# Kernel tuning notes

Hardware: AMD Instinct MI355X
Metric: run time of the kernel (lower is better)

## Reference

```python
import jax, jax.numpy as jnp
import numpy as np

QUERY_SIZE = 512
KEY_SIZE = 512
VALUE_SIZE = 512
HIDDEN = 128


def setup_inputs() -> dict:
    key = jax.random.key(0)
    ks = jax.random.split(key, 9)
    b, t_q, t_k = 8, 128, 512
    query = jax.random.normal(ks[0], (b, t_q, QUERY_SIZE), dtype=jnp.float32)
    keys = jax.random.normal(ks[1], (b, t_k, KEY_SIZE), dtype=jnp.float32)
    values = jax.random.normal(ks[2], (b, t_k, VALUE_SIZE), dtype=jnp.float32)
    # torch nn.Linear init ~ U(-1/sqrt(fan_in), 1/sqrt(fan_in)); scale-matched normals are fine
    sq = 1.0 / np.sqrt(QUERY_SIZE)
    sk = 1.0 / np.sqrt(KEY_SIZE)
    sh = 1.0 / np.sqrt(HIDDEN)
    Wq = jax.random.uniform(ks[3], (HIDDEN, QUERY_SIZE), jnp.float32, -sq, sq)
    bq = jax.random.uniform(ks[4], (HIDDEN,), jnp.float32, -sq, sq)
    Wk = jax.random.uniform(ks[5], (HIDDEN, KEY_SIZE), jnp.float32, -sk, sk)
    bk = jax.random.uniform(ks[6], (HIDDEN,), jnp.float32, -sk, sk)
    Wo = jax.random.uniform(ks[7], (1, HIDDEN), jnp.float32, -sh, sh)
    bo = jax.random.uniform(ks[8], (1,), jnp.float32, -sh, sh)
    return {"query": query, "keys": keys, "values": values,
            "Wq": Wq, "bq": bq, "Wk": Wk, "bk": bk, "Wo": Wo, "bo": bo}


def reference(query, keys, values, Wq, bq, Wk, bk, Wo, bo):
    # Bahdanau additive attention: att_ij = Wo @ tanh(Wq q_i + Wk k_j + bq + bk) + bo
    # Project once per position (mathematically identical to the expanded per-pair Linear).
    q_proj = jnp.einsum('bqn,hn->bqh', query, Wq) + bq          # b x t_q x h
    k_proj = jnp.einsum('bkn,hn->bkh', keys, Wk) + bk           # b x t_k x h
    hid = jnp.tanh(q_proj[:, :, None, :] + k_proj[:, None, :, :])  # b x t_q x t_k x h
    scores = jnp.einsum('bqkh,h->bqk', hid, Wo[0]) + bo[0]       # b x t_q x t_k
    attn = jax.nn.softmax(scores, axis=2)
    context = jnp.einsum('bqk,bkv->bqv', attn, values)           # b x t_q x n_v
    return context, attn
```

## Files before the change

kernel.cpp:

```cpp
#include <hip/hip_runtime.h>


#define B_    8
#define TQ_   128
#define TK_   512
#define NIN_  512
#define H_    128
#define NV_   512
#define NQR   (B_*TQ_)
#define NROWS (NQR + B_*TK_)

#define C2_   2.8853900817779268f
#define L2E_  1.4426950408889634f

__device__ __forceinline__ float fexp2(float x){ return __builtin_amdgcn_exp2f(x); }
__device__ __forceinline__ float frcp (float x){ return __builtin_amdgcn_rcpf(x); }

__global__ __launch_bounds__(128, 4) void proj_kernel(
        const float* __restrict__ query, const float* __restrict__ keys,
        const float* __restrict__ Wq, const float* __restrict__ Wk,
        float* __restrict__ psum, int kper) {
    __shared__ float at[32][20];
    __shared__ float wt[32][132];
    const int tid = threadIdx.x;
    const int r0  = blockIdx.x * 16;
    const float* in; const float* W;
    if (r0 < NQR) { in = query + (size_t)r0 * NIN_;         W = Wq; }
    else          { in = keys  + (size_t)(r0 - NQR) * NIN_; W = Wk; }

    const int r4 = (tid >> 5) * 4;
    const int h4 = (tid & 31) * 4;
    const int sr  = tid >> 3;
    const int skq = (tid & 7) * 4;
    const int kb0 = blockIdx.y * kper;
    const int nc  = kper >> 5;

    const float* pA = in + sr * NIN_ + kb0 + skq;
    const float* pW0 = W + (sr      ) * NIN_ + kb0 + skq;
    const float* pW1 = W + (sr + 16 ) * NIN_ + kb0 + skq;
    const float* pW2 = W + (sr + 32 ) * NIN_ + kb0 + skq;
    const float* pW3 = W + (sr + 48 ) * NIN_ + kb0 + skq;
    const float* pW4 = W + (sr + 64 ) * NIN_ + kb0 + skq;
    const float* pW5 = W + (sr + 80 ) * NIN_ + kb0 + skq;
    const float* pW6 = W + (sr + 96 ) * NIN_ + kb0 + skq;
    const float* pW7 = W + (sr + 112) * NIN_ + kb0 + skq;

    float4 af  = *(const float4*)pA;
    float4 w0 = *(const float4*)pW0, w1 = *(const float4*)pW1;
    float4 w2 = *(const float4*)pW2, w3 = *(const float4*)pW3;
    float4 w4 = *(const float4*)pW4, w5 = *(const float4*)pW5;
    float4 w6 = *(const float4*)pW6, w7 = *(const float4*)pW7;

    float acc[4][4];
#pragma unroll
    for (int i = 0; i < 4; ++i)
#pragma unroll
        for (int j = 0; j < 4; ++j) acc[i][j] = 0.0f;

    for (int c = 0; c < nc; ++c) {
        __syncthreads();
        at[skq+0][sr] = af.x; at[skq+1][sr] = af.y;
        at[skq+2][sr] = af.z; at[skq+3][sr] = af.w;
        wt[skq+0][sr    ] = w0.x; wt[skq+1][sr    ] = w0.y;
        wt[skq+2][sr    ] = w0.z; wt[skq+3][sr    ] = w0.w;
        wt[skq+0][sr+ 16] = w1.x; wt[skq+1][sr+ 16] = w1.y;
        wt[skq+2][sr+ 16] = w1.z; wt[skq+3][sr+ 16] = w1.w;
        wt[skq+0][sr+ 32] = w2.x; wt[skq+1][sr+ 32] = w2.y;
        wt[skq+2][sr+ 32] = w2.z; wt[skq+3][sr+ 32] = w2.w;
        wt[skq+0][sr+ 48] = w3.x; wt[skq+1][sr+ 48] = w3.y;
        wt[skq+2][sr+ 48] = w3.z; wt[skq+3][sr+ 48] = w3.w;
        wt[skq+0][sr+ 64] = w4.x; wt[skq+1][sr+ 64] = w4.y;
        wt[skq+2][sr+ 64] = w4.z; wt[skq+3][sr+ 64] = w4.w;
        wt[skq+0][sr+ 80] = w5.x; wt[skq+1][sr+ 80] = w5.y;
        wt[skq+2][sr+ 80] = w5.z; wt[skq+3][sr+ 80] = w5.w;
        wt[skq+0][sr+ 96] = w6.x; wt[skq+1][sr+ 96] = w6.y;
        wt[skq+2][sr+ 96] = w6.z; wt[skq+3][sr+ 96] = w6.w;
        wt[skq+0][sr+112] = w7.x; wt[skq+1][sr+112] = w7.y;
        wt[skq+2][sr+112] = w7.z; wt[skq+3][sr+112] = w7.w;
        __syncthreads();
        if (c + 1 < nc) {
            pA += 32; pW0 += 32; pW1 += 32; pW2 += 32; pW3 += 32;
            pW4 += 32; pW5 += 32; pW6 += 32; pW7 += 32;
            af = *(const float4*)pA;
            w0 = *(const float4*)pW0; w1 = *(const float4*)pW1;
            w2 = *(const float4*)pW2; w3 = *(const float4*)pW3;
            w4 = *(const float4*)pW4; w5 = *(const float4*)pW5;
            w6 = *(const float4*)pW6; w7 = *(const float4*)pW7;
        }
#pragma unroll 8
        for (int kk = 0; kk < 32; ++kk) {
            float4 a = *(const float4*)&at[kk][r4];
            float4 w = *(const float4*)&wt[kk][h4];
            float av[4] = {a.x, a.y, a.z, a.w};
            float wv[4] = {w.x, w.y, w.z, w.w};
#pragma unroll
            for (int i = 0; i < 4; ++i)
#pragma unroll
                for (int j = 0; j < 4; ++j)
                    acc[i][j] = fmaf(av[i], wv[j], acc[i][j]);
        }
    }

    float* op = psum + ((size_t)blockIdx.y * NROWS + r0) * H_;
#pragma unroll
    for (int i = 0; i < 4; ++i) {
        float4 o = {acc[i][0], acc[i][1], acc[i][2], acc[i][3]};
        *(float4*)&op[(r4 + i) * H_ + h4] = o;
    }
}

__global__ __launch_bounds__(256, 4) void reduce_kernel(
        const float* __restrict__ psum, const float* __restrict__ bq,
        const float* __restrict__ bk, float* __restrict__ qp,
        float* __restrict__ kpT) {
    __shared__ float lt[128][9];
    const int tid = threadIdx.x;
    const int r0  = blockIdx.x * 8;
    const bool isq = (r0 < NQR);
    const float* bias = isq ? bq : bk;

    const int row = tid >> 5, hq = (tid & 31) * 4;
    const float4 b4 = *(const float4*)&bias[hq];
    float4 s = b4;
#pragma unroll
    for (int sp = 0; sp < 4; ++sp) {
        float4 v = *(const float4*)&psum[((size_t)sp * NROWS + r0 + row) * H_ + hq];
        s.x += v.x; s.y += v.y; s.z += v.z; s.w += v.w;
    }
    if (isq) {
        *(float4*)&qp[(size_t)(r0 + row) * H_ + hq] = s;
    } else {
        lt[hq + 0][row] = s.x * C2_; lt[hq + 1][row] = s.y * C2_;
        lt[hq + 2][row] = s.z * C2_; lt[hq + 3][row] = s.w * C2_;
        __syncthreads();
        const int b  = (r0 - NQR) >> 9;
        const int k0 = (r0 - NQR) & 511;
        const int h = tid >> 1, kq = (tid & 1) * 4;
        float4 o = {lt[h][kq], lt[h][kq + 1], lt[h][kq + 2], lt[h][kq + 3]};
        *(float4*)&kpT[((size_t)b * H_ + h) * TK_ + k0 + kq] = o;
    }
}

__global__ __launch_bounds__(256, 4) void scores_kernel(
        const float* __restrict__ qp, const float* __restrict__ kpT,
        const float* __restrict__ Wo, const float* __restrict__ bo,
        float* __restrict__ out_attn) {
    __shared__ float qs2[2][H_];
    __shared__ float w2[H_];
    __shared__ float sc[2][TK_];

    const int tid = threadIdx.x;
    const int b   = blockIdx.y;
    const int q0  = blockIdx.x * 2;
    const int lane = tid & 63;

    qs2[tid >> 7][tid & 127] =
        qp[(b * TQ_ + q0 + (tid >> 7)) * H_ + (tid & 127)] * C2_;
    if (tid < H_) w2[tid] = Wo[tid] * -2.0f;
    __syncthreads();

    float sw = w2[lane] + w2[lane + 64];
#pragma unroll
    for (int m = 1; m < 64; m <<= 1) sw += __shfl_xor(sw, m);
    const float sbase = bo[0] - 0.5f * sw;

    const int k4 = (tid & 127) * 4;
    const int qi = tid >> 7;
    const float* pk = kpT + (size_t)b * H_ * TK_ + k4;
    float a0 = 0.f, a1 = 0.f, a2 = 0.f, a3 = 0.f;
#pragma unroll 4
    for (int h = 0; h < H_; ++h) {
        float4 kv = *(const float4*)pk;
        pk += TK_;
        const float qv = qs2[qi][h];
        const float wv = w2[h];
        a0 = fmaf(wv, frcp(fexp2(qv + kv.x) + 1.0f), a0);
        a1 = fmaf(wv, frcp(fexp2(qv + kv.y) + 1.0f), a1);
        a2 = fmaf(wv, frcp(fexp2(qv + kv.z) + 1.0f), a2);
        a3 = fmaf(wv, frcp(fexp2(qv + kv.w) + 1.0f), a3);
    }
    float4 sv = {a0 + sbase, a1 + sbase, a2 + sbase, a3 + sbase};
    *(float4*)&sc[qi][k4] = sv;
    __syncthreads();

    const int w = tid >> 6;
    if (w < 2) {
        float4 sA = *(const float4*)&sc[w][lane * 8];
        float4 sB = *(const float4*)&sc[w][lane * 8 + 4];
        float m = fmaxf(fmaxf(fmaxf(sA.x, sA.y), fmaxf(sA.z, sA.w)),
                        fmaxf(fmaxf(sB.x, sB.y), fmaxf(sB.z, sB.w)));
#pragma unroll
        for (int mask = 1; mask < 64; mask <<= 1) m = fmaxf(m, __shfl_xor(m, mask));
        float4 eA, eB;
        eA.x = fexp2((sA.x - m) * L2E_); eA.y = fexp2((sA.y - m) * L2E_);
        eA.z = fexp2((sA.z - m) * L2E_); eA.w = fexp2((sA.w - m) * L2E_);
        eB.x = fexp2((sB.x - m) * L2E_); eB.y = fexp2((sB.y - m) * L2E_);
        eB.z = fexp2((sB.z - m) * L2E_); eB.w = fexp2((sB.w - m) * L2E_);
        float s = eA.x + eA.y + eA.z + eA.w + eB.x + eB.y + eB.z + eB.w;
#pragma unroll
        for (int mask = 1; mask < 64; mask <<= 1) s += __shfl_xor(s, mask);
        float inv = frcp(s);
        eA.x *= inv; eA.y *= inv; eA.z *= inv; eA.w *= inv;
        eB.x *= inv; eB.y *= inv; eB.z *= inv; eB.w *= inv;
        float4* op = (float4*)&out_attn[(b * TQ_ + q0 + w) * TK_ + lane * 8];
        op[0] = eA; op[1] = eB;
    }
}

__global__ __launch_bounds__(128, 4) void context_kernel(
        const float* __restrict__ attn, const float* __restrict__ values,
        float* __restrict__ outc) {
    __shared__ float at[32][12];
    __shared__ float vt[32][68];

    const int tid = threadIdx.x;
    const int b   = blockIdx.y;
    const int q0  = (blockIdx.x >> 3) * 8;
    const int v0  = (blockIdx.x & 7) * 64;

    const int v2 = (tid & 31) * 2;
    const int q2 = (tid >> 5) * 2;
    const int ar  = tid >> 3;
    const int akq = (tid & 7) * 4;
    const int vr  = tid >> 4;
    const int vq  = (tid & 15) * 4;

    const float* pAt = attn + (size_t)(b * TQ_ + q0 + ar) * TK_ + akq;
    const float* pV0 = values + (size_t)(b * TK_ + vr     ) * NV_ + v0 + vq;
    const float* pV1 = values + (size_t)(b * TK_ + vr +  8) * NV_ + v0 + vq;
    const float* pV2 = values + (size_t)(b * TK_ + vr + 16) * NV_ + v0 + vq;
    const float* pV3 = values + (size_t)(b * TK_ + vr + 24) * NV_ + v0 + vq;

    float4 af = {0.f,0.f,0.f,0.f};
    if (tid < 64) af = *(const float4*)pAt;
    float4 vf0 = *(const float4*)pV0;
    float4 vf1 = *(const float4*)pV1;
    float4 vf2 = *(const float4*)pV2;
    float4 vf3 = *(const float4*)pV3;

    float acc[2][2] = {{0.f,0.f},{0.f,0.f}};

    for (int c = 0; c < 16; ++c) {
        __syncthreads();
        if (tid < 64) {
            at[akq+0][ar] = af.x; at[akq+1][ar] = af.y;
            at[akq+2][ar] = af.z; at[akq+3][ar] = af.w;
        }
        *(float4*)&vt[vr     ][vq] = vf0;
        *(float4*)&vt[vr +  8][vq] = vf1;
        *(float4*)&vt[vr + 16][vq] = vf2;
        *(float4*)&vt[vr + 24][vq] = vf3;
        __syncthreads();
        if (c + 1 < 16) {
            pAt += 32; pV0 += 32 * NV_; pV1 += 32 * NV_;
            pV2 += 32 * NV_; pV3 += 32 * NV_;
            if (tid < 64) af = *(const float4*)pAt;
            vf0 = *(const float4*)pV0; vf1 = *(const float4*)pV1;
            vf2 = *(const float4*)pV2; vf3 = *(const float4*)pV3;
        }
#pragma unroll 8
        for (int kk = 0; kk < 32; ++kk) {
            float2 a = *(const float2*)&at[kk][q2];
            float2 v = *(const float2*)&vt[kk][v2];
            acc[0][0] = fmaf(a.x, v.x, acc[0][0]);
            acc[0][1] = fmaf(a.x, v.y, acc[0][1]);
            acc[1][0] = fmaf(a.y, v.x, acc[1][0]);
            acc[1][1] = fmaf(a.y, v.y, acc[1][1]);
        }
    }
    float2 o0 = {acc[0][0], acc[0][1]};
    float2 o1 = {acc[1][0], acc[1][1]};
    *(float2*)&outc[(size_t)(b * TQ_ + q0 + q2 + 0) * NV_ + v0 + v2] = o0;
    *(float2*)&outc[(size_t)(b * TQ_ + q0 + q2 + 1) * NV_ + v0 + v2] = o1;
}

extern "C" void kernel_launch(void* const* d_in, const int* in_sizes, int n_in,
                              void* d_out, int out_size, void* d_ws, size_t ws_size,
                              hipStream_t stream) {
    const float* query  = (const float*)d_in[0];
    const float* keys   = (const float*)d_in[1];
    const float* values = (const float*)d_in[2];
    const float* Wq     = (const float*)d_in[3];
    const float* bq     = (const float*)d_in[4];
    const float* Wk     = (const float*)d_in[5];
    const float* bk     = (const float*)d_in[6];
    const float* Wo     = (const float*)d_in[7];
    const float* bo     = (const float*)d_in[8];

    float* out_ctx  = (float*)d_out;
    float* out_attn = out_ctx + B_ * TQ_ * NV_;
    float* qp   = (float*)d_ws;
    float* kpT  = qp + (size_t)NQR * H_;
    float* psum = kpT + (size_t)B_ * H_ * TK_;

    proj_kernel<<<dim3(NROWS / 16, 4), 128, 0, stream>>>(
        query, keys, Wq, Wk, psum, NIN_ / 4);
    reduce_kernel<<<NROWS / 8, 256, 0, stream>>>(psum, bq, bk, qp, kpT);
    scores_kernel<<<dim3(TQ_ / 2, B_), 256, 0, stream>>>(qp, kpT, Wo, bo, out_attn);
    context_kernel<<<dim3(128, B_), 128, 0, stream>>>(out_attn, values, out_ctx);
}
```

Measured before the change: 69.17 us.

## Drop split-K reduce kernel, fuse bias into projection, row-major key layout in scores

The projection kernel no longer splits the 512-wide reduction four ways. Each block now computes the full K for 16 rows and 64 hidden units, then adds the bias and C2 scale directly, so the separate reduce kernel and its partial-sum traffic are gone. Keys are stored row-major and not transposed. The scores kernel now has each thread handle one key with both queries, reading contiguous float4s of kp and broadcast q and w from shared memory. The cost is fewer, longer projection blocks, and strided per-thread kp reads in scores that may coalesce poorly.

```diff
diff --git a/kernel.cpp b/kernel.cpp
--- a/kernel.cpp
+++ b/kernel.cpp
@@ -18,131 +18,86 @@
 
 __global__ __launch_bounds__(128, 4) void proj_kernel(
         const float* __restrict__ query, const float* __restrict__ keys,
-        const float* __restrict__ Wq, const float* __restrict__ Wk,
-        float* __restrict__ psum, int kper) {
+        const float* __restrict__ Wq, const float* __restrict__ bq,
+        const float* __restrict__ Wk, const float* __restrict__ bk,
+        float* __restrict__ qp, float* __restrict__ kp) {
     __shared__ float at[32][20];
-    __shared__ float wt[32][132];
+    __shared__ float wt[32][68];
     const int tid = threadIdx.x;
-    const int r0  = blockIdx.x * 16;
-    const float* in; const float* W;
-    if (r0 < NQR) { in = query + (size_t)r0 * NIN_;         W = Wq; }
-    else          { in = keys  + (size_t)(r0 - NQR) * NIN_; W = Wk; }
-
-    const int r4 = (tid >> 5) * 4;
-    const int h4 = (tid & 31) * 4;
+    const int r0  = (blockIdx.x >> 1) * 16;
+    const int h0  = (blockIdx.x & 1) * 64;
+    const float* in; const float* W; const float* bias; float* outp;
+    if (r0 < NQR) {
+        in = query + (size_t)r0 * NIN_; W = Wq; bias = bq;
+        outp = qp + (size_t)r0 * H_;
+    } else {
+        const int rk = r0 - NQR;
+        in = keys + (size_t)rk * NIN_;  W = Wk; bias = bk;
+        outp = kp + (size_t)rk * H_;
+    }
+
+    const int r2  = (tid >> 4) * 2;
+    const int h4l = (tid & 15) * 4;
     const int sr  = tid >> 3;
     const int skq = (tid & 7) * 4;
-    const int kb0 = blockIdx.y * kper;
-    const int nc  = kper >> 5;
-
-    const float* pA = in + sr * NIN_ + kb0 + skq;
-    const float* pW0 = W + (sr      ) * NIN_ + kb0 + skq;
-    const float* pW1 = W + (sr + 16 ) * NIN_ + kb0 + skq;
-    const float* pW2 = W + (sr + 32 ) * NIN_ + kb0 + skq;
-    const float* pW3 = W + (sr + 48 ) * NIN_ + kb0 + skq;
-    const float* pW4 = W + (sr + 64 ) * NIN_ + kb0 + skq;
-    const float* pW5 = W + (sr + 80 ) * NIN_ + kb0 + skq;
-    const float* pW6 = W + (sr + 96 ) * NIN_ + kb0 + skq;
-    const float* pW7 = W + (sr + 112) * NIN_ + kb0 + skq;
-
-    float4 af  = *(const float4*)pA;
+
+    const float* pA  = in + (size_t)sr * NIN_ + skq;
+    const float* pW0 = W + (size_t)(h0 + sr     ) * NIN_ + skq;
+    const float* pW1 = W + (size_t)(h0 + sr + 16) * NIN_ + skq;
+    const float* pW2 = W + (size_t)(h0 + sr + 32) * NIN_ + skq;
+    const float* pW3 = W + (size_t)(h0 + sr + 48) * NIN_ + skq;
+
+    float4 af = *(const float4*)pA;
     float4 w0 = *(const float4*)pW0, w1 = *(const float4*)pW1;
     float4 w2 = *(const float4*)pW2, w3 = *(const float4*)pW3;
-    float4 w4 = *(const float4*)pW4, w5 = *(const float4*)pW5;
-    float4 w6 = *(const float4*)pW6, w7 = *(const float4*)pW7;
-
-    float acc[4][4];
-#pragma unroll
-    for (int i = 0; i < 4; ++i)
-#pragma unroll
-        for (int j = 0; j < 4; ++j) acc[i][j] = 0.0f;
-
-    for (int c = 0; c < nc; ++c) {
+
+    float acc[2][4] = {{0.f,0.f,0.f,0.f},{0.f,0.f,0.f,0.f}};
+
+    for (int c = 0; c < 16; ++c) {
         __syncthreads();
         at[skq+0][sr] = af.x; at[skq+1][sr] = af.y;
         at[skq+2][sr] = af.z; at[skq+3][sr] = af.w;
-        wt[skq+0][sr    ] = w0.x; wt[skq+1][sr    ] = w0.y;
-        wt[skq+2][sr    ] = w0.z; wt[skq+3][sr    ] = w0.w;
-        wt[skq+0][sr+ 16] = w1.x; wt[skq+1][sr+ 16] = w1.y;
-        wt[skq+2][sr+ 16] = w1.z; wt[skq+3][sr+ 16] = w1.w;
-        wt[skq+0][sr+ 32] = w2.x; wt[skq+1][sr+ 32] = w2.y;
-        wt[skq+2][sr+ 32] = w2.z; wt[skq+3][sr+ 32] = w2.w;
-        wt[skq+0][sr+ 48] = w3.x; wt[skq+1][sr+ 48] = w3.y;
-        wt[skq+2][sr+ 48] = w3.z; wt[skq+3][sr+ 48] = w3.w;
-        wt[skq+0][sr+ 64] = w4.x; wt[skq+1][sr+ 64] = w4.y;
-        wt[skq+2][sr+ 64] = w4.z; wt[skq+3][sr+ 64] = w4.w;
-        wt[skq+0][sr+ 80] = w5.x; wt[skq+1][sr+ 80] = w5.y;
-        wt[skq+2][sr+ 80] = w5.z; wt[skq+3][sr+ 80] = w5.w;
-        wt[skq+0][sr+ 96] = w6.x; wt[skq+1][sr+ 96] = w6.y;
-        wt[skq+2][sr+ 96] = w6.z; wt[skq+3][sr+ 96] = w6.w;
-        wt[skq+0][sr+112] = w7.x; wt[skq+1][sr+112] = w7.y;
-        wt[skq+2][sr+112] = w7.z; wt[skq+3][sr+112] = w7.w;
-        __syncthreads();
-        if (c + 1 < nc) {
+        wt[skq+0][sr   ] = w0.x; wt[skq+1][sr   ] = w0.y;
+        wt[skq+2][sr   ] = w0.z; wt[skq+3][sr   ] = w0.w;
+        wt[skq+0][sr+16] = w1.x; wt[skq+1][sr+16] = w1.y;
+        wt[skq+2][sr+16] = w1.z; wt[skq+3][sr+16] = w1.w;
+        wt[skq+0][sr+32] = w2.x; wt[skq+1][sr+32] = w2.y;
+        wt[skq+2][sr+32] = w2.z; wt[skq+3][sr+32] = w2.w;
+        wt[skq+0][sr+48] = w3.x; wt[skq+1][sr+48] = w3.y;
+        wt[skq+2][sr+48] = w3.z; wt[skq+3][sr+48] = w3.w;
+        __syncthreads();
+        if (c + 1 < 16) {
             pA += 32; pW0 += 32; pW1 += 32; pW2 += 32; pW3 += 32;
-            pW4 += 32; pW5 += 32; pW6 += 32; pW7 += 32;
             af = *(const float4*)pA;
             w0 = *(const float4*)pW0; w1 = *(const float4*)pW1;
             w2 = *(const float4*)pW2; w3 = *(const float4*)pW3;
-            w4 = *(const float4*)pW4; w5 = *(const float4*)pW5;
-            w6 = *(const float4*)pW6; w7 = *(const float4*)pW7;
         }
 #pragma unroll 8
         for (int kk = 0; kk < 32; ++kk) {
-            float4 a = *(const float4*)&at[kk][r4];
-            float4 w = *(const float4*)&wt[kk][h4];
-            float av[4] = {a.x, a.y, a.z, a.w};
-            float wv[4] = {w.x, w.y, w.z, w.w};
-#pragma unroll
-            for (int i = 0; i < 4; ++i)
-#pragma unroll
-                for (int j = 0; j < 4; ++j)
-                    acc[i][j] = fmaf(av[i], wv[j], acc[i][j]);
-        }
-    }
-
-    float* op = psum + ((size_t)blockIdx.y * NROWS + r0) * H_;
-#pragma unroll
-    for (int i = 0; i < 4; ++i) {
-        float4 o = {acc[i][0], acc[i][1], acc[i][2], acc[i][3]};
-        *(float4*)&op[(r4 + i) * H_ + h4] = o;
-    }
-}
-
-__global__ __launch_bounds__(256, 4) void reduce_kernel(
-        const float* __restrict__ psum, const float* __restrict__ bq,
-        const float* __restrict__ bk, float* __restrict__ qp,
-        float* __restrict__ kpT) {
-    __shared__ float lt[128][9];
-    const int tid = threadIdx.x;
-    const int r0  = blockIdx.x * 8;
-    const bool isq = (r0 < NQR);
-    const float* bias = isq ? bq : bk;
-
-    const int row = tid >> 5, hq = (tid & 31) * 4;
-    const float4 b4 = *(const float4*)&bias[hq];
-    float4 s = b4;
-#pragma unroll
-    for (int sp = 0; sp < 4; ++sp) {
-        float4 v = *(const float4*)&psum[((size_t)sp * NROWS + r0 + row) * H_ + hq];
-        s.x += v.x; s.y += v.y; s.z += v.z; s.w += v.w;
-    }
-    if (isq) {
-        *(float4*)&qp[(size_t)(r0 + row) * H_ + hq] = s;
-    } else {
-        lt[hq + 0][row] = s.x * C2_; lt[hq + 1][row] = s.y * C2_;
-        lt[hq + 2][row] = s.z * C2_; lt[hq + 3][row] = s.w * C2_;
-        __syncthreads();
-        const int b  = (r0 - NQR) >> 9;
-        const int k0 = (r0 - NQR) & 511;
-        const int h = tid >> 1, kq = (tid & 1) * 4;
-        float4 o = {lt[h][kq], lt[h][kq + 1], lt[h][kq + 2], lt[h][kq + 3]};
-        *(float4*)&kpT[((size_t)b * H_ + h) * TK_ + k0 + kq] = o;
+            const float2 a = *(const float2*)&at[kk][r2];
+            const float4 w = *(const float4*)&wt[kk][h4l];
+            acc[0][0] = fmaf(a.x, w.x, acc[0][0]);
+            acc[0][1] = fmaf(a.x, w.y, acc[0][1]);
+            acc[0][2] = fmaf(a.x, w.z, acc[0][2]);
+            acc[0][3] = fmaf(a.x, w.w, acc[0][3]);
+            acc[1][0] = fmaf(a.y, w.x, acc[1][0]);
+            acc[1][1] = fmaf(a.y, w.y, acc[1][1]);
+            acc[1][2] = fmaf(a.y, w.z, acc[1][2]);
+            acc[1][3] = fmaf(a.y, w.w, acc[1][3]);
+        }
+    }
+
+    const float4 b4 = *(const float4*)&bias[h0 + h4l];
+#pragma unroll
+    for (int i = 0; i < 2; ++i) {
+        float4 o = {(acc[i][0] + b4.x) * C2_, (acc[i][1] + b4.y) * C2_,
+                    (acc[i][2] + b4.z) * C2_, (acc[i][3] + b4.w) * C2_};
+        *(float4*)&outp[(size_t)(r2 + i) * H_ + h0 + h4l] = o;
     }
 }
 
 __global__ __launch_bounds__(256, 4) void scores_kernel(
-        const float* __restrict__ qp, const float* __restrict__ kpT,
+        const float* __restrict__ qp, const float* __restrict__ kp,
         const float* __restrict__ Wo, const float* __restrict__ bo,
         float* __restrict__ out_attn) {
     __shared__ float qs2[2][H_];
@@ -155,7 +110,7 @@
     const int lane = tid & 63;
 
     qs2[tid >> 7][tid & 127] =
-        qp[(b * TQ_ + q0 + (tid >> 7)) * H_ + (tid & 127)] * C2_;
+        qp[(size_t)(b * TQ_ + q0 + (tid >> 7)) * H_ + (tid & 127)];
     if (tid < H_) w2[tid] = Wo[tid] * -2.0f;
     __syncthreads();
 
@@ -164,23 +119,29 @@
     for (int m = 1; m < 64; m <<= 1) sw += __shfl_xor(sw, m);
     const float sbase = bo[0] - 0.5f * sw;
 
-    const int k4 = (tid & 127) * 4;
-    const int qi = tid >> 7;
-    const float* pk = kpT + (size_t)b * H_ * TK_ + k4;
-    float a0 = 0.f, a1 = 0.f, a2 = 0.f, a3 = 0.f;
+#pragma unroll
+    for (int half = 0; half < 2; ++half) {
+        const int k = tid + half * 256;
+        const float4* kp4 = (const float4*)&kp[(size_t)(b * TK_ + k) * H_];
+        float s0 = 0.f, s1 = 0.f;
 #pragma unroll 4
-    for (int h = 0; h < H_; ++h) {
-        float4 kv = *(const float4*)pk;
-        pk += TK_;
-        const float qv = qs2[qi][h];
-        const float wv = w2[h];
-        a0 = fmaf(wv, frcp(fexp2(qv + kv.x) + 1.0f), a0);
-        a1 = fmaf(wv, frcp(fexp2(qv + kv.y) + 1.0f), a1);
-        a2 = fmaf(wv, frcp(fexp2(qv + kv.z) + 1.0f), a2);
-        a3 = fmaf(wv, frcp(fexp2(qv + kv.w) + 1.0f), a3);
-    }
-    float4 sv = {a0 + sbase, a1 + sbase, a2 + sbase, a3 + sbase};
-    *(float4*)&sc[qi][k4] = sv;
+        for (int hb = 0; hb < 32; ++hb) {
+            const float4 kv  = kp4[hb];
+            const float4 wv  = *(const float4*)&w2[hb * 4];
+            const float4 q0v = *(const float4*)&qs2[0][hb * 4];
+            const float4 q1v = *(const float4*)&qs2[1][hb * 4];
+            s0 = fmaf(wv.x, frcp(fexp2(q0v.x + kv.x) + 1.f), s0);
+            s0 = fmaf(wv.y, frcp(fexp2(q0v.y + kv.y) + 1.f), s0);
+            s0 = fmaf(wv.z, frcp(fexp2(q0v.z + kv.z) + 1.f), s0);
+            s0 = fmaf(wv.w, frcp(fexp2(q0v.w + kv.w) + 1.f), s0);
+            s1 = fmaf(wv.x, frcp(fexp2(q1v.x + kv.x) + 1.f), s1);
+            s1 = fmaf(wv.y, frcp(fexp2(q1v.y + kv.y) + 1.f), s1);
+            s1 = fmaf(wv.z, frcp(fexp2(q1v.z + kv.z) + 1.f), s1);
+            s1 = fmaf(wv.w, frcp(fexp2(q1v.w + kv.w) + 1.f), s1);
+        }
+        sc[0][k] = s0 + sbase;
+        sc[1][k] = s1 + sbase;
+    }
     __syncthreads();
 
     const int w = tid >> 6;
@@ -190,7 +151,7 @@
         float m = fmaxf(fmaxf(fmaxf(sA.x, sA.y), fmaxf(sA.z, sA.w)),
                         fmaxf(fmaxf(sB.x, sB.y), fmaxf(sB.z, sB.w)));
 #pragma unroll
-        for (int mask = 1; mask < 64; mask <<= 1) m = fmaxf(m, __shfl_xor(m, mask));
+        for (int mk = 1; mk < 64; mk <<= 1) m = fmaxf(m, __shfl_xor(m, mk));
         float4 eA, eB;
         eA.x = fexp2((sA.x - m) * L2E_); eA.y = fexp2((sA.y - m) * L2E_);
         eA.z = fexp2((sA.z - m) * L2E_); eA.w = fexp2((sA.w - m) * L2E_);
@@ -198,11 +159,11 @@
         eB.z = fexp2((sB.z - m) * L2E_); eB.w = fexp2((sB.w - m) * L2E_);
         float s = eA.x + eA.y + eA.z + eA.w + eB.x + eB.y + eB.z + eB.w;
 #pragma unroll
-        for (int mask = 1; mask < 64; mask <<= 1) s += __shfl_xor(s, mask);
-        float inv = frcp(s);
+        for (int mk = 1; mk < 64; mk <<= 1) s += __shfl_xor(s, mk);
+        const float inv = frcp(s);
         eA.x *= inv; eA.y *= inv; eA.z *= inv; eA.w *= inv;
         eB.x *= inv; eB.y *= inv; eB.z *= inv; eB.w *= inv;
-        float4* op = (float4*)&out_attn[(b * TQ_ + q0 + w) * TK_ + lane * 8];
+        float4* op = (float4*)&out_attn[(size_t)(b * TQ_ + q0 + w) * TK_ + lane * 8];
         op[0] = eA; op[1] = eB;
     }
 }
@@ -260,8 +221,8 @@
         }
 #pragma unroll 8
         for (int kk = 0; kk < 32; ++kk) {
-            float2 a = *(const float2*)&at[kk][q2];
-            float2 v = *(const float2*)&vt[kk][v2];
+            const float2 a = *(const float2*)&at[kk][q2];
+            const float2 v = *(const float2*)&vt[kk][v2];
             acc[0][0] = fmaf(a.x, v.x, acc[0][0]);
             acc[0][1] = fmaf(a.x, v.y, acc[0][1]);
             acc[1][0] = fmaf(a.y, v.x, acc[1][0]);
@@ -289,13 +250,11 @@
 
     float* out_ctx  = (float*)d_out;
     float* out_attn = out_ctx + B_ * TQ_ * NV_;
-    float* qp   = (float*)d_ws;
-    float* kpT  = qp + (size_t)NQR * H_;
-    float* psum = kpT + (size_t)B_ * H_ * TK_;
-
-    proj_kernel<<<dim3(NROWS / 16, 4), 128, 0, stream>>>(
-        query, keys, Wq, Wk, psum, NIN_ / 4);
-    reduce_kernel<<<NROWS / 8, 256, 0, stream>>>(psum, bq, bk, qp, kpT);
-    scores_kernel<<<dim3(TQ_ / 2, B_), 256, 0, stream>>>(qp, kpT, Wo, bo, out_attn);
+    float* qp = (float*)d_ws;
+    float* kp = qp + (size_t)NQR * H_;
+
+    proj_kernel<<<dim3(NROWS / 16 * 2), 128, 0, stream>>>(
+        query, keys, Wq, bq, Wk, bk, qp, kp);
+    scores_kernel<<<dim3(TQ_ / 2, B_), 256, 0, stream>>>(qp, kp, Wo, bo, out_attn);
     context_kernel<<<dim3(128, B_), 128, 0, stream>>>(out_attn, values, out_ctx);
 }
```

Measured after the change: 72.14 us. +4.3%, slower.
